# Optimization experiments

Measured on AMD Instinct MI355X. Metric: run time of the kernel, lower is better.

## Reference

```python
import jax, jax.numpy as jnp
import numpy as np

EPS = 1e-6
BN_EPS = 1e-5


def point_cells(loc_orig, H, W):
    # map [-1,1] xy coords to nearest cell index on an HxW grid
    loc = jnp.clip(loc_orig, -1.0, 1.0) * 0.5 + 0.5
    cx = jnp.clip(jnp.round(loc[..., 0] * (W - 1)), 0, W - 1).astype(jnp.int32)
    cy = jnp.clip(jnp.round(loc[..., 1] * (H - 1)), 0, H - 1).astype(jnp.int32)
    return cx + cy * W  # (B, N0)


def token2map(x, loc_orig, idx_agg, H, W):
    # scatter token features to an HxW map, averaging per cell
    B, N, C = x.shape
    N0 = loc_orig.shape[1]
    cell = point_cells(loc_orig, H, W)                      # (B, N0)
    feat = jnp.take_along_axis(x, idx_agg[..., None], axis=1)  # (B, N0, C)
    flat = (cell + jnp.arange(B)[:, None] * (H * W)).reshape(-1)
    s = jax.ops.segment_sum(feat.reshape(-1, C), flat, num_segments=B * H * W)
    cnt = jax.ops.segment_sum(jnp.ones((B * N0,), x.dtype), flat, num_segments=B * H * W)
    x_map = s / (cnt[:, None] + EPS)
    return x_map.reshape(B, H, W, C)


def map2token(x_map, N, loc_orig, idx_agg, agg_weight):
    # gather map features at original point locations, aggregate per token
    B, H, W, C = x_map.shape
    cell = point_cells(loc_orig, H, W)
    feat = jnp.take_along_axis(x_map.reshape(B, H * W, C), cell[..., None], axis=1)  # (B, N0, C)
    v = agg_weight.reshape(B, -1, 1)
    tflat = (idx_agg + jnp.arange(B)[:, None] * N).reshape(-1)
    s = jax.ops.segment_sum((feat * v).reshape(-1, C), tflat, num_segments=B * N)
    norm = jax.ops.segment_sum(v.reshape(-1), tflat, num_segments=B * N)
    return (s / (norm[:, None] + EPS)).reshape(B, N, C)


def token_cluster_grid(x, loc_orig, idx_agg, weight, H, W):
    # merge tokens into an (H//2)x(W//2) grid with confidence-weighted averaging
    B, N, C = x.shape
    H2, W2 = H // 2, W // 2
    Ns = H2 * W2
    cell = point_cells(loc_orig, H2, W2)                           # (B, N0) new token per point
    v = jnp.take_along_axis(weight, idx_agg[..., None], axis=1)     # (B, N0, 1)
    feat = jnp.take_along_axis(x, idx_agg[..., None], axis=1)       # (B, N0, C)
    flat = (cell + jnp.arange(B)[:, None] * Ns).reshape(-1)
    s = jax.ops.segment_sum((feat * v).reshape(-1, C), flat, num_segments=B * Ns)
    norm = jax.ops.segment_sum(v.reshape(-1), flat, num_segments=B * Ns) + EPS
    x_down = (s / norm[:, None]).reshape(B, Ns, C)
    weight_t = (v.reshape(-1) / norm[flat]).reshape(B, -1, 1)       # per-point normalized weight
    return x_down, cell, weight_t


def reference(x, loc_orig, idx_agg, agg_weight, conv_w, conv_b, skip_w, bn_gamma, bn_beta, conf_w, conf_b, H, W):
    B, N, C = x.shape
    x_map = token2map(x, loc_orig, idx_agg, H, W)  # (B, H, W, C)
    y = jax.lax.conv_general_dilated(
        x_map, conv_w, window_strides=(2, 2), padding=((1, 1), (1, 1)),
        dimension_numbers=('NHWC', 'HWIO', 'NHWC')) + conv_b  # (B, H/2, W/2, dim_out)
    xt = map2token(y, N, loc_orig, idx_agg, agg_weight) + x @ skip_w  # (B, N, dim_out)
    # BatchNorm over (B, N) per channel (training-mode batch stats)
    mean = jnp.mean(xt, axis=(0, 1))
    var = jnp.var(xt, axis=(0, 1))
    xt = (xt - mean) * jax.lax.rsqrt(var + BN_EPS) * bn_gamma + bn_beta
    conf = xt @ conf_w + conf_b          # (B, N, 1)
    weight = jnp.exp(conf)
    x_down, idx_agg_down, weight_t = token_cluster_grid(xt, loc_orig, idx_agg, weight, H, W)
    agg_weight_down = agg_weight * weight_t
    agg_weight_down = agg_weight_down / jnp.max(agg_weight_down, axis=1, keepdims=True)
    x_down = jax.nn.relu(x_down)
    x_act = jax.nn.relu(xt)
    return x_down, idx_agg_down, agg_weight_down, x_act, conf


def setup_inputs() -> dict:
    key = jax.random.key(0)
    ks = jax.random.split(key, 8)
    B, N, C, Cout, H, W = 64, 4096, 64, 128, 64, 64
    x = jax.random.normal(ks[0], (B, N, C), dtype=jnp.float32)
    loc_orig = jax.random.uniform(ks[1], (B, N, 2), dtype=jnp.float32, minval=-1.0, maxval=1.0)
    idx_agg = jax.random.randint(ks[2], (B, N), 0, N, dtype=jnp.int32)
    agg_weight = jax.random.uniform(ks[3], (B, N, 1), dtype=jnp.float32, minval=0.1, maxval=1.0)
    conv_w = jax.random.normal(ks[4], (3, 3, C, Cout), dtype=jnp.float32) * (1.0 / np.sqrt(9 * C))
    conv_b = jnp.zeros((Cout,), jnp.float32)
    skip_w = jax.random.normal(ks[5], (C, Cout), dtype=jnp.float32) * (1.0 / np.sqrt(C))
    bn_gamma = jnp.ones((Cout,), jnp.float32)
    bn_beta = jnp.zeros((Cout,), jnp.float32)
    conf_w = jax.random.normal(ks[6], (Cout, 1), dtype=jnp.float32) * (1.0 / np.sqrt(Cout))
    conf_b = jnp.zeros((1,), jnp.float32)
    return {"x": x, "loc_orig": loc_orig, "idx_agg": idx_agg, "agg_weight": agg_weight,
            "conv_w": conv_w, "conv_b": conv_b, "skip_w": skip_w,
            "bn_gamma": bn_gamma, "bn_beta": bn_beta, "conf_w": conf_w, "conf_b": conf_b,
            "H": H, "W": W}
```

## Files before the change

kernel.cpp:

```cpp
#include <hip/hip_runtime.h>

#define BB 64
#define NN 4096
#define CCH 64
#define CO 128
#define HH 64
#define WW 64
#define H2 32
#define W2 32
#define EPSF 1e-6f
#define BNEPS 1e-5f

typedef unsigned short ushort_t;
using bf8  = __attribute__((ext_vector_type(8))) short;
using f32x4 = __attribute__((ext_vector_type(4))) float;

__device__ inline ushort_t f2bf(float f) {
  unsigned u = __float_as_uint(f);
  unsigned r = (u + 0x7fffu + ((u >> 16) & 1u)) >> 16;
  return (ushort_t)r;
}
__device__ inline float bflo(unsigned u) { return __uint_as_float(u << 16); }
__device__ inline float bfhi(unsigned u) { return __uint_as_float(u & 0xffff0000u); }

__device__ inline void gload_lds16(const void* src, void* ldsdst) {
  __builtin_amdgcn_global_load_lds((const __attribute__((address_space(1))) void*)src,
                                   (__attribute__((address_space(3))) void*)ldsdst, 16, 0, 0);
}

__device__ inline void cells_from_loc(float lx, float ly, int& c64, int& c32) {
  lx = fminf(fmaxf(lx, -1.f), 1.f) * 0.5f + 0.5f;
  ly = fminf(fmaxf(ly, -1.f), 1.f) * 0.5f + 0.5f;
  int cx = (int)fminf(fmaxf(rintf(lx * (WW - 1)), 0.f), (float)(WW - 1));
  int cy = (int)fminf(fmaxf(rintf(ly * (HH - 1)), 0.f), (float)(HH - 1));
  c64 = cx + cy * WW;
  int cx2 = (int)fminf(fmaxf(rintf(lx * (W2 - 1)), 0.f), (float)(W2 - 1));
  int cy2 = (int)fminf(fmaxf(rintf(ly * (H2 - 1)), 0.f), (float)(H2 - 1));
  c32 = cx2 + cy2 * W2;
}

__global__ __launch_bounds__(256) void k_zero(uint4* __restrict__ p) {
  p[blockIdx.x * 256 + threadIdx.x] = make_uint4(0u, 0u, 0u, 0u);
}

__global__ __launch_bounds__(256) void k_prep(const float* __restrict__ loc, const int* __restrict__ idxagg,
                                              const float* __restrict__ aw,
                                              float* __restrict__ idx_out,
                                              unsigned* __restrict__ pck64, unsigned* __restrict__ pck32,
                                              unsigned* __restrict__ pckT, float* __restrict__ nrm) {
  int i = blockIdx.x * 256 + threadIdx.x;
  int b = i >> 12;
  int c64, c2;
  cells_from_loc(loc[2 * i], loc[2 * i + 1], c64, c2);
  idx_out[i] = (float)c2;
  atomicAdd(&pck64[(b << 12) + c64], 1u);
  atomicAdd(&pck32[(b << 10) + c2], 1u);
  atomicAdd(&pckT[(b << 12) + idxagg[i]], 1u);
  unsafeAtomicAdd(&nrm[(b << 12) + idxagg[i]], aw[i]);
}

__global__ __launch_bounds__(256) void k_wprep(const float* __restrict__ convw, const float* __restrict__ skipw,
                                               ushort_t* __restrict__ wT, ushort_t* __restrict__ swT) {
  int e = blockIdx.x * 256 + threadIdx.x;
  if (e < 9 * CCH * CO) {
    int co = e & 127, k = e >> 7;
    wT[co * 576 + k] = f2bf(convw[k * CO + co]);
  } else {
    int e2 = e - 9 * CCH * CO;
    int co = e2 & 127, k = e2 >> 7;
    swT[co * 64 + k] = f2bf(skipw[k * CO + co]);
  }
}

__device__ void block_exscan_pack(unsigned* __restrict__ buf, int L) {
  __shared__ int partial[256];
  int tid = threadIdx.x;
  int per = L >> 8;
  int base = tid * per;
  int s = 0;
  for (int i = 0; i < per; i++) s += (int)buf[base + i];
  __syncthreads();
  partial[tid] = s;
  __syncthreads();
  for (int d = 1; d < 256; d <<= 1) {
    int v = (tid >= d) ? partial[tid - d] : 0;
    __syncthreads();
    partial[tid] += v;
    __syncthreads();
  }
  int run = (tid == 0) ? 0 : partial[tid - 1];
  for (int i = 0; i < per; i++) {
    int n = (int)buf[base + i];
    buf[base + i] = ((unsigned)run << 16) | (unsigned)run;
    run += n;
  }
}

__global__ __launch_bounds__(256) void k_scan(unsigned* __restrict__ pck64, unsigned* __restrict__ pckT,
                                              unsigned* __restrict__ pck32) {
  int b = blockIdx.x / 3, kind = blockIdx.x - 3 * (blockIdx.x / 3);
  if (kind == 0)      block_exscan_pack(pck64 + ((size_t)b << 12), 4096);
  else if (kind == 1) block_exscan_pack(pckT + ((size_t)b << 12), 4096);
  else                block_exscan_pack(pck32 + ((size_t)b << 10), 1024);
}

__global__ __launch_bounds__(256) void k_fill(const float* __restrict__ loc, const int* __restrict__ idxagg,
                                              const float* __restrict__ aw,
                                              unsigned* __restrict__ pck64, unsigned* __restrict__ pckT,
                                              unsigned* __restrict__ pck32,
                                              ushort_t* __restrict__ list64, unsigned* __restrict__ listT,
                                              unsigned* __restrict__ list32) {
  int i = blockIdx.x * 256 + threadIdx.x;
  int b = i >> 12, p = i & 4095;
  int c64, c2;
  cells_from_loc(loc[2 * i], loc[2 * i + 1], c64, c2);
  int idx = idxagg[i];
  unsigned pos = atomicAdd(&pck64[(b << 12) + c64], 1u) & 0xffffu;
  list64[(b << 12) + pos] = (ushort_t)idx;
  pos = atomicAdd(&pckT[(b << 12) + idx], 1u) & 0xffffu;
  listT[(b << 12) + pos] = ((unsigned)c2 << 16) | (unsigned)f2bf(aw[i]);
  pos = atomicAdd(&pck32[(b << 10) + c2], 1u) & 0xffffu;
  list32[(b << 12) + pos] = ((unsigned)idx << 16) | (unsigned)p;
}

__global__ __launch_bounds__(256) void k_border(ushort_t* __restrict__ xmb) {
  int t = blockIdx.x * 256 + threadIdx.x;
  int q = t & 15;
  int cell = (t >> 4) % 260;
  int b = t / (260 * 16);
  int r, c;
  if (cell < 66)       { r = 0;  c = cell; }
  else if (cell < 132) { r = 65; c = cell - 66; }
  else if (cell < 196) { r = cell - 132 + 1; c = 0; }
  else                 { r = cell - 196 + 1; c = 65; }
  *(uint2*)&xmb[(((size_t)(b * 66 + r)) * 66 + c) * 64 + q * 4] = make_uint2(0u, 0u);
}

__global__ __launch_bounds__(256) void k_t2m(const float* __restrict__ x,
                                             const unsigned* __restrict__ pck64,
                                             const ushort_t* __restrict__ list64, ushort_t* __restrict__ xmb) {
  int blk = blockIdx.x;
  int xcd = blk & 7, lblk = blk >> 3;
  int wave = threadIdx.x >> 6, lane = threadIdx.x & 63;
  int cbase = xcd * 32768 + lblk * 32 + wave * 8;
#pragma unroll 1
  for (int k = 0; k < 8; k++) {
    int g = cbase + k;
    int b = g >> 12, cell = g & 4095;
    unsigned v = pck64[g];
    int o = (int)(v >> 16), n = (int)(v & 0xffffu) - o;
    const ushort_t* lp = list64 + ((size_t)b << 12) + o;
    const float* xb = x + ((size_t)b << 18);
    float s0 = 0.f, s1 = 0.f, s2 = 0.f, s3 = 0.f;
    int i = 0;
    for (; i + 4 <= n; i += 4) {
      int i0 = lp[i], i1 = lp[i + 1], i2 = lp[i + 2], i3 = lp[i + 3];
      s0 += xb[(size_t)i0 * 64 + lane];
      s1 += xb[(size_t)i1 * 64 + lane];
      s2 += xb[(size_t)i2 * 64 + lane];
      s3 += xb[(size_t)i3 * 64 + lane];
    }
    for (; i < n; i++) s0 += xb[(size_t)lp[i] * 64 + lane];
    float avg = (s0 + s1 + s2 + s3) / ((float)n + EPSF);
    int r = cell >> 6, cc = cell & 63;
    xmb[(((size_t)(b * 66 + r + 1)) * 66 + cc + 1) * 64 + lane] = f2bf(avg);
  }
}

__global__ __launch_bounds__(256) void k_conv(const ushort_t* __restrict__ xmb, const ushort_t* __restrict__ wT,
                                              const float* __restrict__ cb, ushort_t* __restrict__ y) {
  __shared__ ushort_t A[2][4096];
  const int tid = threadIdx.x;
  const int wave = tid >> 6, lane = tid & 63;
  const int m0 = blockIdx.x * 128;

  f32x4 acc[2][8];
  {
    float bv[8];
#pragma unroll
    for (int nt = 0; nt < 8; nt++) bv[nt] = cb[nt * 16 + (lane & 15)];
#pragma unroll
    for (int mt = 0; mt < 2; mt++)
#pragma unroll
      for (int nt = 0; nt < 8; nt++) {
        f32x4 a; a[0] = bv[nt]; a[1] = bv[nt]; a[2] = bv[nt]; a[3] = bv[nt];
        acc[mt][nt] = a;
      }
  }

  const int srcslot = (((lane & 3) ^ ((lane >> 3) & 3))) * 8;
  int sb[2], soy[2], sox[2];
#pragma unroll
  for (int q = 0; q < 2; q++) {
    int r = wave * 32 + q * 16 + (lane >> 2);
    int s = m0 + r;
    sb[q] = s >> 10; soy[q] = (s >> 5) & 31; sox[q] = s & 31;
  }

  auto stage = [&](int ks, int buf) {
    int kp = ks >> 1, ci0 = (ks & 1) * 32;
    int ky = kp / 3, kx = kp - ky * 3;
#pragma unroll
    for (int q = 0; q < 2; q++) {
      int iy = 2 * soy[q] + ky, ix = 2 * sox[q] + kx;
      const ushort_t* src = xmb + (((size_t)sb[q] * 66 + iy) * 66 + ix) * 64 + ci0 + srcslot;
      gload_lds16(src, &A[buf][(wave * 32 + q * 16) * 32]);
    }
  };

  stage(0, 0);
  const int rdslotx = (lane >> 1) & 3;
  for (int ks = 0; ks < 18; ks++) {
    int buf = ks & 1;
    __syncthreads();
    if (ks < 17) stage(ks + 1, buf ^ 1);
    bf8 a[2];
#pragma unroll
    for (int mt = 0; mt < 2; mt++) {
      int r = wave * 32 + mt * 16 + (lane & 15);
      int slot = (lane >> 4) ^ rdslotx;
      a[mt] = *(const bf8*)&A[buf][r * 32 + slot * 8];
    }
    int k0 = ks * 32 + (lane >> 4) * 8;
#pragma unroll
    for (int nt = 0; nt < 8; nt++) {
      int co = nt * 16 + (lane & 15);
      bf8 bbf = *(const bf8*)&wT[co * 576 + k0];
      acc[0][nt] = __builtin_amdgcn_mfma_f32_16x16x32_bf16(a[0], bbf, acc[0][nt], 0, 0, 0);
      acc[1][nt] = __builtin_amdgcn_mfma_f32_16x16x32_bf16(a[1], bbf, acc[1][nt], 0, 0, 0);
    }
  }
#pragma unroll
  for (int mt = 0; mt < 2; mt++)
#pragma unroll
    for (int nt = 0; nt < 8; nt++) {
      int co = nt * 16 + (lane & 15);
#pragma unroll
      for (int j = 0; j < 4; j++) {
        int srow = m0 + wave * 32 + mt * 16 + (lane >> 4) * 4 + j;
        y[(size_t)srow * 128 + co] = f2bf(acc[mt][nt][j]);
      }
    }
}

__global__ __launch_bounds__(256) void k_xt(const float* __restrict__ x, const ushort_t* __restrict__ swT,
                                            const ushort_t* __restrict__ y,
                                            const unsigned* __restrict__ listT, const unsigned* __restrict__ pckT,
                                            const float* __restrict__ nrm,
                                            ushort_t* __restrict__ XTB, float* __restrict__ BNP) {
  __shared__ float xg[64 * 128];
  __shared__ float nrminv[64];
  __shared__ float bnred[256];
  const int tid = threadIdx.x, wave = tid >> 6, lane = tid & 63;
  int blk = blockIdx.x;
  int sblk = (blk & 7) * 512 + (blk >> 3);
  const int t0 = sblk * 64;
  const int b = t0 >> 12, lt0 = t0 & 4095;

#pragma unroll
  for (int q = 0; q < 4; q++) {
    int ch = wave * 4 + q;
    int r = ch * 4 + (lane >> 4);
    int sp = lane & 15;
    const float* src = x + ((size_t)(t0 + r)) * 64 + ((sp ^ (r & 7)) << 2);
    gload_lds16(src, (char*)xg + ch * 1024);
  }
  if (tid < 64) nrminv[tid] = 1.f / (nrm[(b << 12) + lt0 + tid] + EPSF);
  bnred[tid] = 0.f;
  __syncthreads();

  bf8 afr[2];
  {
    int r = wave * 16 + (lane & 15);
#pragma unroll
    for (int ks = 0; ks < 2; ks++) {
      int cs = ks * 4 + (lane >> 4);
      const float4 f0 = *(const float4*)&xg[r * 64 + (((2 * cs) ^ (r & 7)) << 2)];
      const float4 f1 = *(const float4*)&xg[r * 64 + (((2 * cs + 1) ^ (r & 7)) << 2)];
      bf8 v;
      v[0] = (short)f2bf(f0.x); v[1] = (short)f2bf(f0.y);
      v[2] = (short)f2bf(f0.z); v[3] = (short)f2bf(f0.w);
      v[4] = (short)f2bf(f1.x); v[5] = (short)f2bf(f1.y);
      v[6] = (short)f2bf(f1.z); v[7] = (short)f2bf(f1.w);
      afr[ks] = v;
    }
  }

  f32x4 acc[8];
#pragma unroll
  for (int nt = 0; nt < 8; nt++) { f32x4 z; z[0] = 0; z[1] = 0; z[2] = 0; z[3] = 0; acc[nt] = z; }
#pragma unroll
  for (int ks = 0; ks < 2; ks++)
#pragma unroll
    for (int nt = 0; nt < 8; nt++) {
      int co = nt * 16 + (lane & 15);
      bf8 bbf = *(const bf8*)&swT[co * 64 + ks * 32 + (lane >> 4) * 8];
      acc[nt] = __builtin_amdgcn_mfma_f32_16x16x32_bf16(afr[ks], bbf, acc[nt], 0, 0, 0);
    }

  __syncthreads();

#pragma unroll
  for (int rr = 0; rr < 16; rr++) {
    *(float2*)&xg[(wave * 16 + rr) * 128 + ((2 * lane) ^ ((rr & 7) << 4))] = make_float2(0.f, 0.f);
  }

  {
    int gtok = lt0 + wave * 16 + lane;
    int myoff = 0;
    if (lane <= 16) myoff = (gtok >= NN) ? NN : (int)(pckT[(b << 12) + gtok] >> 16);
    int pbeg = __shfl(myoff, 0, 64), pend = __shfl(myoff, 16, 64);
    const unsigned* ltb = listT + ((size_t)b << 12);
    const ushort_t* yb = y + ((size_t)b << 17);
    for (int chunk = pbeg; chunk < pend; chunk += 64) {
      int pid = chunk + lane;
      unsigned rec = 0u;
      if (pid < pend) rec = ltb[pid];
      int rr = 0;
#pragma unroll
      for (int j = 1; j <= 16; j++) rr += (pid >= __shfl(myoff, j, 64)) ? 1 : 0;
      int nrec = min(64, pend - chunk);
      int i = 0;
      for (; i + 4 <= nrec; i += 4) {
        unsigned yu[4]; float vv[4]; int rw[4];
#pragma unroll
        for (int u = 0; u < 4; u++) {
          unsigned rb = (unsigned)__shfl((int)rec, i + u, 64);
          vv[u] = __uint_as_float(rb << 16);
          rw[u] = __shfl(rr, i + u, 64);
          yu[u] = *(const unsigned*)&yb[(size_t)(rb >> 16) * 128 + lane * 2];
        }
#pragma unroll
        for (int u = 0; u < 4; u++) {
          float2* p = (float2*)&xg[(wave * 16 + rw[u]) * 128 + ((2 * lane) ^ ((rw[u] & 7) << 4))];
          float2 cv = *p;
          cv.x += bflo(yu[u]) * vv[u]; cv.y += bfhi(yu[u]) * vv[u];
          *p = cv;
        }
      }
      for (; i < nrec; i++) {
        unsigned rb = (unsigned)__shfl((int)rec, i, 64);
        float v = __uint_as_float(rb << 16);
        int rw0 = __shfl(rr, i, 64);
        unsigned yu0 = *(const unsigned*)&yb[(size_t)(rb >> 16) * 128 + lane * 2];
        float2* p = (float2*)&xg[(wave * 16 + rw0) * 128 + ((2 * lane) ^ ((rw0 & 7) << 4))];
        float2 cv = *p;
        cv.x += bflo(yu0) * v; cv.y += bfhi(yu0) * v;
        *p = cv;
      }
    }
  }

#pragma unroll
  for (int nt = 0; nt < 8; nt++) {
    int co = nt * 16 + (lane & 15);
    float s = 0.f, q = 0.f;
#pragma unroll
    for (int j = 0; j < 4; j++) {
      int r = wave * 16 + (lane >> 4) * 4 + j;
      float val = acc[nt][j] + xg[r * 128 + (co ^ ((r & 7) << 4))] * nrminv[r];
      acc[nt][j] = val;
      s += val; q += val * val;
    }
    s += __shfl_xor(s, 16, 64); s += __shfl_xor(s, 32, 64);
    q += __shfl_xor(q, 16, 64); q += __shfl_xor(q, 32, 64);
    if (lane < 16) {
      atomicAdd(&bnred[nt * 16 + lane], s);
      atomicAdd(&bnred[128 + nt * 16 + lane], q);
    }
  }
  __syncthreads();

  ushort_t* xto = (ushort_t*)xg;
#pragma unroll
  for (int nt = 0; nt < 8; nt++) {
    int co = nt * 16 + (lane & 15);
#pragma unroll
    for (int j = 0; j < 4; j++) {
      int r = wave * 16 + (lane >> 4) * 4 + j;
      xto[r * 128 + (co ^ ((r & 7) << 4))] = f2bf(acc[nt][j]);
    }
  }
  __syncthreads();
#pragma unroll
  for (int it = 0; it < 4; it++) {
    int q8 = (it * 256 + tid) * 8;
    int r = q8 >> 7, c = q8 & 127;
    uint4 vv = *(const uint4*)&xto[r * 128 + (c ^ ((r & 7) << 4))];
    *(uint4*)&XTB[((size_t)t0) * 128 + q8] = vv;
  }
  unsafeAtomicAdd(&BNP[(blk & 63) * 256 + tid], bnred[tid]);
}

__global__ void k_bnfin(const float* __restrict__ BNP, const float* __restrict__ gamma,
                        const float* __restrict__ beta, float* __restrict__ ss) {
  int c = threadIdx.x;
  float s = 0.f, q = 0.f;
#pragma unroll 4
  for (int k = 0; k < 64; k++) {
    s += BNP[k * 256 + c];
    q += BNP[k * 256 + 128 + c];
  }
  float n = (float)(BB * NN);
  float mean = s / n;
  float var = q / n - mean * mean;
  float sc = gamma[c] * rsqrtf(var + BNEPS);
  ss[c] = sc;
  ss[128 + c] = beta[c] - mean * sc;
}

__global__ __launch_bounds__(256) void k_conf(const ushort_t* __restrict__ XTB, const float* __restrict__ ss,
                                              const float* __restrict__ confw, const float* __restrict__ confb,
                                              float* __restrict__ conf_out, float* __restrict__ wgt,
                                              float* __restrict__ xa) {
  int blk = blockIdx.x;
  int xcd = blk & 7, lblk = blk >> 3;
  int l32 = threadIdx.x & 31, tok8 = threadIdx.x >> 5;
  int c0 = l32 * 4;
  const float4 sc = *(const float4*)&ss[c0];
  const float4 sh = *(const float4*)&ss[128 + c0];
  const float4 cw = *(const float4*)&confw[c0];
  const float cb0 = confb[0];
#pragma unroll 1
  for (int pass = 0; pass < 4; pass++) {
    int p = xcd * 32768 + lblk * 32 + pass * 8 + tok8;
    const uint2 pw = *(const uint2*)&XTB[(size_t)p * 128 + c0];
    float v0 = bflo(pw.x) * sc.x + sh.x;
    float v1 = bfhi(pw.x) * sc.y + sh.y;
    float v2 = bflo(pw.y) * sc.z + sh.z;
    float v3 = bfhi(pw.y) * sc.w + sh.w;
    float4 xo;
    xo.x = fmaxf(v0, 0.f); xo.y = fmaxf(v1, 0.f);
    xo.z = fmaxf(v2, 0.f); xo.w = fmaxf(v3, 0.f);
    *(float4*)&xa[(size_t)p * 128 + c0] = xo;
    float s = v0 * cw.x + v1 * cw.y + v2 * cw.z + v3 * cw.w;
#pragma unroll
    for (int off = 16; off; off >>= 1) s += __shfl_down(s, off, 32);
    if (l32 == 0) {
      float cf = s + cb0;
      conf_out[p] = cf;
      wgt[p] = __expf(cf);
    }
  }
}

__global__ __launch_bounds__(256) void k_cluster(const ushort_t* __restrict__ XTB, const float* __restrict__ ss,
                                                 const float* __restrict__ wgt, const float* __restrict__ aw,
                                                 const unsigned* __restrict__ pck32,
                                                 const unsigned* __restrict__ list32,
                                                 float* __restrict__ xd, float* __restrict__ awd,
                                                 int* __restrict__ maxb) {
  __shared__ float smax[4];
  int blk = blockIdx.x;
  int xcd = blk & 7, lblk = blk >> 3;
  int wave = threadIdx.x >> 6, lane = threadIdx.x & 63;
  int wbase = xcd * 8192 + lblk * 16 + wave * 4;
  int b = wbase >> 10;
  const float* wb = wgt + ((size_t)b << 12);
  const float* awb = aw + ((size_t)b << 12);
  const ushort_t* xtb = XTB + (((size_t)b) << 19);
  const float2 sc = *(const float2*)&ss[2 * lane];
  const float2 sh = *(const float2*)&ss[128 + 2 * lane];
  float mymax = 0.f;
#pragma unroll 1
  for (int k = 0; k < 4; k++) {
    int wid = wbase + k;
    unsigned v = pck32[wid];
    int o = (int)(v >> 16), n = (int)(v & 0xffffu) - o;
    const unsigned* lp = list32 + ((size_t)b << 12) + o;
    float s0 = 0.f, s1 = 0.f, sv = 0.f;
    int i = 0;
    for (; i + 2 <= n; i += 2) {
      unsigned r0 = lp[i], r1 = lp[i + 1];
      int i0 = r0 >> 16, i1 = r1 >> 16;
      float v0 = wb[i0], v1 = wb[i1];
      unsigned p0 = *(const unsigned*)&xtb[(size_t)i0 * 128 + 2 * lane];
      unsigned p1 = *(const unsigned*)&xtb[(size_t)i1 * 128 + 2 * lane];
      s0 += (bflo(p0) * sc.x + sh.x) * v0 + (bflo(p1) * sc.x + sh.x) * v1;
      s1 += (bfhi(p0) * sc.y + sh.y) * v0 + (bfhi(p1) * sc.y + sh.y) * v1;
      sv += v0 + v1;
    }
    if (i < n) {
      unsigned r0 = lp[i];
      int i0 = r0 >> 16;
      float v0 = wb[i0];
      unsigned p0 = *(const unsigned*)&xtb[(size_t)i0 * 128 + 2 * lane];
      s0 += (bflo(p0) * sc.x + sh.x) * v0;
      s1 += (bfhi(p0) * sc.y + sh.y) * v0;
      sv += v0;
    }
    float inv = 1.f / (sv + EPSF);
    float2 o2; o2.x = fmaxf(s0 * inv, 0.f); o2.y = fmaxf(s1 * inv, 0.f);
    *(float2*)&xd[(size_t)wid * 128 + 2 * lane] = o2;

    for (int kk = lane; kk < n; kk += 64) {
      unsigned rec = lp[kk];
      int idx = rec >> 16, pp = rec & 0xffffu;
      float a = awb[pp] * wb[idx] * inv;
      awd[(b << 12) + pp] = a;
      mymax = fmaxf(mymax, a);
    }
  }
#pragma unroll
  for (int off = 32; off; off >>= 1) mymax = fmaxf(mymax, __shfl_down(mymax, off, 64));
  if (lane == 0) smax[wave] = mymax;
  __syncthreads();
  if (threadIdx.x == 0) {
    float m = fmaxf(fmaxf(smax[0], smax[1]), fmaxf(smax[2], smax[3]));
    atomicMax(&maxb[b], __float_as_int(m));
  }
}

__global__ __launch_bounds__(256) void k_awdnorm(float* __restrict__ awd, const int* __restrict__ maxb) {
  int p = blockIdx.x * 256 + threadIdx.x;
  int b = p >> 12;
  awd[p] = awd[p] / __int_as_float(maxb[b]);
}

extern "C" void kernel_launch(void* const* d_in, const int* in_sizes, int n_in,
                              void* d_out, int out_size, void* d_ws, size_t ws_size,
                              hipStream_t stream) {
  (void)in_sizes; (void)n_in; (void)out_size;
  const float* x      = (const float*)d_in[0];
  const float* loc    = (const float*)d_in[1];
  const int*   idxagg = (const int*)  d_in[2];
  const float* aw     = (const float*)d_in[3];
  const float* convw  = (const float*)d_in[4];
  const float* convb  = (const float*)d_in[5];
  const float* skipw  = (const float*)d_in[6];
  const float* gamma  = (const float*)d_in[7];
  const float* beta   = (const float*)d_in[8];
  const float* confw  = (const float*)d_in[9];
  const float* confb  = (const float*)d_in[10];

  char* ws = (char*)d_ws;
  ushort_t* XTB   = (ushort_t*)(ws + 0);
  ushort_t* XMB   = (ushort_t*)(ws + 0);
  ushort_t* Y     = (ushort_t*)(ws + 67108864);
  ushort_t* WT    = (ushort_t*)(ws + 83886080);
  ushort_t* SWT   = (ushort_t*)(ws + 84033536);
  unsigned* PCK64 = (unsigned*)(ws + 84049920);
  unsigned* PCKT  = (unsigned*)(ws + 85098496);
  unsigned* PCK32 = (unsigned*)(ws + 86147072);
  float*    NRM   = (float*)  (ws + 86409216);
  float*    BNP   = (float*)  (ws + 87457792);
  int*      MAXB  = (int*)    (ws + 87523328);
  ushort_t* LIST64= (ushort_t*)(ws + 87524352);
  unsigned* LISTT = (unsigned*)(ws + 88048640);
  unsigned* LIST32= (unsigned*)(ws + 89097216);
  float*    WGT   = (float*)  (ws + 90145792);
  float*    SS    = (float*)  (ws + 91194368);
  if (ws_size < 91195392) return;

  float* out    = (float*)d_out;
  float* O_XD   = out;
  float* O_IDX  = out + 8388608;
  float* O_AWD  = out + 8650752;
  float* XA     = out + 8912896;
  float* O_CONF = out + 42467328;

  k_zero   <<<849,   256, 0, stream>>>((uint4*)(ws + 84049920));
  k_prep   <<<1024,  256, 0, stream>>>(loc, idxagg, aw, O_IDX, PCK64, PCK32, PCKT, NRM);
  k_wprep  <<<320,   256, 0, stream>>>(convw, skipw, WT, SWT);
  k_scan   <<<192,   256, 0, stream>>>(PCK64, PCKT, PCK32);
  k_fill   <<<1024,  256, 0, stream>>>(loc, idxagg, aw, PCK64, PCKT, PCK32, LIST64, LISTT, LIST32);
  k_border <<<1040,  256, 0, stream>>>(XMB);
  k_t2m    <<<8192,  256, 0, stream>>>(x, PCK64, LIST64, XMB);
  k_conv   <<<512,   256, 0, stream>>>(XMB, WT, convb, Y);
  k_xt     <<<4096,  256, 0, stream>>>(x, SWT, Y, LISTT, PCKT, NRM, XTB, BNP);
  k_bnfin  <<<1,     128, 0, stream>>>(BNP, gamma, beta, SS);
  k_conf   <<<8192,  256, 0, stream>>>(XTB, SS, confw, confb, O_CONF, WGT, XA);
  k_cluster<<<4096,  256, 0, stream>>>(XTB, SS, WGT, aw, PCK32, LIST32, O_XD, O_AWD, MAXB);
  k_awdnorm<<<1024,  256, 0, stream>>>(O_AWD, MAXB);
}
```

Before: 339.4 us.

## Merge weight-prep and border kernels into neighbors; preload index lists via shuffles

Measured after the change: 346.3 us. 1.02x slower.

```diff
diff --git a/kernel.cpp b/kernel.cpp
--- a/kernel.cpp
+++ b/kernel.cpp
@@ -47,8 +47,23 @@
                                               const float* __restrict__ aw,
                                               float* __restrict__ idx_out,
                                               unsigned* __restrict__ pck64, unsigned* __restrict__ pck32,
-                                              unsigned* __restrict__ pckT, float* __restrict__ nrm) {
-  int i = blockIdx.x * 256 + threadIdx.x;
+                                              unsigned* __restrict__ pckT, float* __restrict__ nrm,
+                                              const float* __restrict__ convw, const float* __restrict__ skipw,
+                                              ushort_t* __restrict__ wT, ushort_t* __restrict__ swT) {
+  int blk = blockIdx.x;
+  if (blk >= 1024) {
+    int e = (blk - 1024) * 256 + threadIdx.x;
+    if (e < 9 * CCH * CO) {
+      int co = e & 127, k = e >> 7;
+      wT[co * 576 + k] = f2bf(convw[k * CO + co]);
+    } else {
+      int e2 = e - 9 * CCH * CO;
+      int co = e2 & 127, k = e2 >> 7;
+      swT[co * 64 + k] = f2bf(skipw[k * CO + co]);
+    }
+    return;
+  }
+  int i = blk * 256 + threadIdx.x;
   int b = i >> 12;
   int c64, c2;
   cells_from_loc(loc[2 * i], loc[2 * i + 1], c64, c2);
@@ -59,19 +74,6 @@
   unsafeAtomicAdd(&nrm[(b << 12) + idxagg[i]], aw[i]);
 }
 
-__global__ __launch_bounds__(256) void k_wprep(const float* __restrict__ convw, const float* __restrict__ skipw,
-                                               ushort_t* __restrict__ wT, ushort_t* __restrict__ swT) {
-  int e = blockIdx.x * 256 + threadIdx.x;
-  if (e < 9 * CCH * CO) {
-    int co = e & 127, k = e >> 7;
-    wT[co * 576 + k] = f2bf(convw[k * CO + co]);
-  } else {
-    int e2 = e - 9 * CCH * CO;
-    int co = e2 & 127, k = e2 >> 7;
-    swT[co * 64 + k] = f2bf(skipw[k * CO + co]);
-  }
-}
-
 __device__ void block_exscan_pack(unsigned* __restrict__ buf, int L) {
   __shared__ int partial[256];
   int tid = threadIdx.x;
@@ -109,8 +111,22 @@
                                               unsigned* __restrict__ pck64, unsigned* __restrict__ pckT,
                                               unsigned* __restrict__ pck32,
                                               ushort_t* __restrict__ list64, unsigned* __restrict__ listT,
-                                              unsigned* __restrict__ list32) {
-  int i = blockIdx.x * 256 + threadIdx.x;
+                                              unsigned* __restrict__ list32, ushort_t* __restrict__ xmb) {
+  int blk = blockIdx.x;
+  if (blk >= 1024) {
+    int t = (blk - 1024) * 256 + threadIdx.x;
+    int q = t & 15;
+    int cell = (t >> 4) % 260;
+    int b = t / (260 * 16);
+    int r, c;
+    if (cell < 66)       { r = 0;  c = cell; }
+    else if (cell < 132) { r = 65; c = cell - 66; }
+    else if (cell < 196) { r = cell - 132 + 1; c = 0; }
+    else                 { r = cell - 196 + 1; c = 65; }
+    *(uint2*)&xmb[(((size_t)(b * 66 + r)) * 66 + c) * 64 + q * 4] = make_uint2(0u, 0u);
+    return;
+  }
+  int i = blk * 256 + threadIdx.x;
   int b = i >> 12, p = i & 4095;
   int c64, c2;
   cells_from_loc(loc[2 * i], loc[2 * i + 1], c64, c2);
@@ -123,19 +139,6 @@
   list32[(b << 12) + pos] = ((unsigned)idx << 16) | (unsigned)p;
 }
 
-__global__ __launch_bounds__(256) void k_border(ushort_t* __restrict__ xmb) {
-  int t = blockIdx.x * 256 + threadIdx.x;
-  int q = t & 15;
-  int cell = (t >> 4) % 260;
-  int b = t / (260 * 16);
-  int r, c;
-  if (cell < 66)       { r = 0;  c = cell; }
-  else if (cell < 132) { r = 65; c = cell - 66; }
-  else if (cell < 196) { r = cell - 132 + 1; c = 0; }
-  else                 { r = cell - 196 + 1; c = 65; }
-  *(uint2*)&xmb[(((size_t)(b * 66 + r)) * 66 + c) * 64 + q * 4] = make_uint2(0u, 0u);
-}
-
 __global__ __launch_bounds__(256) void k_t2m(const float* __restrict__ x,
                                              const unsigned* __restrict__ pck64,
                                              const ushort_t* __restrict__ list64, ushort_t* __restrict__ xmb) {
@@ -143,25 +146,39 @@
   int xcd = blk & 7, lblk = blk >> 3;
   int wave = threadIdx.x >> 6, lane = threadIdx.x & 63;
   int cbase = xcd * 32768 + lblk * 32 + wave * 8;
+  int b = cbase >> 12;
+  unsigned pcks[8];
+  *(uint4*)&pcks[0] = *(const uint4*)&pck64[cbase];
+  *(uint4*)&pcks[4] = *(const uint4*)&pck64[cbase + 4];
+  int o0 = (int)(pcks[0] >> 16);
+  int total = (int)(pcks[7] & 0xffffu) - o0;
+  const ushort_t* lp0 = list64 + ((size_t)b << 12) + o0;
+  int myrec = (lane < total) ? (int)lp0[lane] : 0;
+  const float* xb = x + ((size_t)b << 18);
 #pragma unroll 1
   for (int k = 0; k < 8; k++) {
-    int g = cbase + k;
-    int b = g >> 12, cell = g & 4095;
-    unsigned v = pck64[g];
-    int o = (int)(v >> 16), n = (int)(v & 0xffffu) - o;
-    const ushort_t* lp = list64 + ((size_t)b << 12) + o;
-    const float* xb = x + ((size_t)b << 18);
+    int off = (int)(pcks[k] >> 16) - o0;
+    int n = (int)(pcks[k] & 0xffffu) - (int)(pcks[k] >> 16);
     float s0 = 0.f, s1 = 0.f, s2 = 0.f, s3 = 0.f;
     int i = 0;
     for (; i + 4 <= n; i += 4) {
-      int i0 = lp[i], i1 = lp[i + 1], i2 = lp[i + 2], i3 = lp[i + 3];
+      int j = off + i;
+      int i0 = (j     < 64) ? __shfl(myrec, j,     64) : (int)lp0[j];
+      int i1 = (j + 1 < 64) ? __shfl(myrec, j + 1, 64) : (int)lp0[j + 1];
+      int i2 = (j + 2 < 64) ? __shfl(myrec, j + 2, 64) : (int)lp0[j + 2];
+      int i3 = (j + 3 < 64) ? __shfl(myrec, j + 3, 64) : (int)lp0[j + 3];
       s0 += xb[(size_t)i0 * 64 + lane];
       s1 += xb[(size_t)i1 * 64 + lane];
       s2 += xb[(size_t)i2 * 64 + lane];
       s3 += xb[(size_t)i3 * 64 + lane];
     }
-    for (; i < n; i++) s0 += xb[(size_t)lp[i] * 64 + lane];
+    for (; i < n; i++) {
+      int j = off + i;
+      int i0 = (j < 64) ? __shfl(myrec, j, 64) : (int)lp0[j];
+      s0 += xb[(size_t)i0 * 64 + lane];
+    }
     float avg = (s0 + s1 + s2 + s3) / ((float)n + EPSF);
+    int cell = (cbase + k) & 4095;
     int r = cell >> 6, cc = cell & 63;
     xmb[(((size_t)(b * 66 + r + 1)) * 66 + cc + 1) * 64 + lane] = f2bf(avg);
   }
@@ -257,6 +274,12 @@
   const int t0 = sblk * 64;
   const int b = t0 >> 12, lt0 = t0 & 4095;
 
+  int myoff = 0;
+  {
+    int gtok = lt0 + wave * 16 + lane;
+    if (lane <= 16) myoff = (gtok >= NN) ? NN : (int)(pckT[(b << 12) + gtok] >> 16);
+  }
+
 #pragma unroll
   for (int q = 0; q < 4; q++) {
     int ch = wave * 4 + q;
@@ -300,22 +323,20 @@
 
   __syncthreads();
 
+  int pbeg = __shfl(myoff, 0, 64), pend = __shfl(myoff, 16, 64);
+  const unsigned* ltb = listT + ((size_t)b << 12);
+  unsigned rec = (pbeg + lane < pend) ? ltb[pbeg + lane] : 0u;
 #pragma unroll
   for (int rr = 0; rr < 16; rr++) {
     *(float2*)&xg[(wave * 16 + rr) * 128 + ((2 * lane) ^ ((rr & 7) << 4))] = make_float2(0.f, 0.f);
   }
 
   {
-    int gtok = lt0 + wave * 16 + lane;
-    int myoff = 0;
-    if (lane <= 16) myoff = (gtok >= NN) ? NN : (int)(pckT[(b << 12) + gtok] >> 16);
-    int pbeg = __shfl(myoff, 0, 64), pend = __shfl(myoff, 16, 64);
-    const unsigned* ltb = listT + ((size_t)b << 12);
     const ushort_t* yb = y + ((size_t)b << 17);
     for (int chunk = pbeg; chunk < pend; chunk += 64) {
       int pid = chunk + lane;
-      unsigned rec = 0u;
-      if (pid < pend) rec = ltb[pid];
+      unsigned currec = rec;
+      if (chunk + 64 < pend) rec = (pid + 64 < pend) ? ltb[pid + 64] : 0u;
       int rr = 0;
 #pragma unroll
       for (int j = 1; j <= 16; j++) rr += (pid >= __shfl(myoff, j, 64)) ? 1 : 0;
@@ -325,7 +346,7 @@
         unsigned yu[4]; float vv[4]; int rw[4];
 #pragma unroll
         for (int u = 0; u < 4; u++) {
-          unsigned rb = (unsigned)__shfl((int)rec, i + u, 64);
+          unsigned rb = (unsigned)__shfl((int)currec, i + u, 64);
           vv[u] = __uint_as_float(rb << 16);
           rw[u] = __shfl(rr, i + u, 64);
           yu[u] = *(const unsigned*)&yb[(size_t)(rb >> 16) * 128 + lane * 2];
@@ -339,7 +360,7 @@
         }
       }
       for (; i < nrec; i++) {
-        unsigned rb = (unsigned)__shfl((int)rec, i, 64);
+        unsigned rb = (unsigned)__shfl((int)currec, i, 64);
         float v = __uint_as_float(rb << 16);
         int rw0 = __shfl(rr, i, 64);
         unsigned yu0 = *(const unsigned*)&yb[(size_t)(rb >> 16) * 128 + lane * 2];
@@ -560,11 +581,10 @@
   float* O_CONF = out + 42467328;
 
   k_zero   <<<849,   256, 0, stream>>>((uint4*)(ws + 84049920));
-  k_prep   <<<1024,  256, 0, stream>>>(loc, idxagg, aw, O_IDX, PCK64, PCK32, PCKT, NRM);
-  k_wprep  <<<320,   256, 0, stream>>>(convw, skipw, WT, SWT);
+  k_prep   <<<1344,  256, 0, stream>>>(loc, idxagg, aw, O_IDX, PCK64, PCK32, PCKT, NRM,
+                                       convw, skipw, WT, SWT);
   k_scan   <<<192,   256, 0, stream>>>(PCK64, PCKT, PCK32);
-  k_fill   <<<1024,  256, 0, stream>>>(loc, idxagg, aw, PCK64, PCKT, PCK32, LIST64, LISTT, LIST32);
-  k_border <<<1040,  256, 0, stream>>>(XMB);
+  k_fill   <<<2064,  256, 0, stream>>>(loc, idxagg, aw, PCK64, PCKT, PCK32, LIST64, LISTT, LIST32, XMB);
   k_t2m    <<<8192,  256, 0, stream>>>(x, PCK64, LIST64, XMB);
   k_conv   <<<512,   256, 0, stream>>>(XMB, WT, convb, Y);
   k_xt     <<<4096,  256, 0, stream>>>(x, SWT, Y, LISTT, PCKT, NRM, XTB, BNP);
```
